# Performance work log

Measured on AMD Instinct MI355X. Metric: run time of the kernel, lower is better.

## Reference

```python
import jax, jax.numpy as jnp
import numpy as np

N_NODES = 100000
N_EDGES = 3200000
FEAT = 16


def gcn_conv(x, src, dst, W, b):
    # PyG GCNConv: add self-loops, symmetric normalization deg^{-1/2}(A+I)deg^{-1/2},
    # then linear transform and scatter-add aggregation.
    n = x.shape[0]
    loop = jnp.arange(n, dtype=src.dtype)
    s = jnp.concatenate([src, loop])
    d = jnp.concatenate([dst, loop])
    deg = jax.ops.segment_sum(jnp.ones_like(d, dtype=x.dtype), d, num_segments=n)
    dinv = jnp.where(deg > 0, jax.lax.rsqrt(deg), 0.0)
    norm = dinv[s] * dinv[d]  # [E+N]
    h = x @ W  # [N, out]
    msg = h[s] * norm[:, None]  # gather + weight
    out = jax.ops.segment_sum(msg, d, num_segments=n)  # scatter-add
    return out + b


def setup_inputs() -> dict:
    key = jax.random.key(0)
    k1, k2, k3, k4 = jax.random.split(key, 4)
    scale = 1.0 / np.sqrt(FEAT)
    return {
        "x": jax.random.normal(k1, (N_NODES, FEAT), dtype=jnp.float32),
        "edge_index": jax.random.randint(k2, (2, N_EDGES), 0, N_NODES, dtype=jnp.int64) if jax.config.jax_enable_x64 else jax.random.randint(k2, (2, N_EDGES), 0, N_NODES, dtype=jnp.int32),
        "W1": jax.random.normal(k3, (FEAT, 16), dtype=jnp.float32) * scale,
        "b1": jnp.zeros((16,), dtype=jnp.float32),
        "W2": jax.random.normal(k4, (16, FEAT), dtype=jnp.float32) * scale,
        "b2": jnp.zeros((FEAT,), dtype=jnp.float32),
    }


def reference(x, edge_index, W1, b1, W2, b2):
    src, dst = edge_index[0], edge_index[1]
    h = gcn_conv(x, src, dst, W1, b1)
    h = jax.nn.relu(h)
    out = gcn_conv(h, src, dst, W2, b2)
    return out
```

## Files before the change

### kernel.cpp

```cpp
#include <hip/hip_runtime.h>

#define F 16
#define BSHIFT 8
#define NPB 256
#define NB 391
#define CH 4096
#define BCAP 9216


__global__ void init_cursor_kernel(unsigned* __restrict__ cursor) {
    int i = threadIdx.x;
    if (i < NB) cursor[i * 16] = (unsigned)(i * BCAP);
}

__global__ __launch_bounds__(512) void
reorder_kernel(const int* __restrict__ src, const int* __restrict__ dst,
               unsigned* __restrict__ cursor, unsigned* __restrict__ recs, int E) {
    __shared__ unsigned lsorted[CH];
    __shared__ unsigned short lbkt[CH];
    __shared__ unsigned cnt[NB];
    __shared__ unsigned lstart[NB + 1];
    int t = threadIdx.x, b = blockIdx.x;
    int e0 = b * CH;
    int cnt_e = E - e0; if (cnt_e > CH) cnt_e = CH;

    for (int i = t; i < NB; i += 512) cnt[i] = 0;
    __syncthreads();
    unsigned pk[8], rs[8];
#pragma unroll
    for (int j = 0; j < 8; ++j) {
        int i = t + j * 512;
        pk[j] = 0xFFFFFFFFu;
        if (i < cnt_e) {
            unsigned d = (unsigned)dst[e0 + i];
            rs[j] = (unsigned)src[e0 + i];
            unsigned bk = d >> BSHIFT;
            unsigned r = atomicAdd(&cnt[bk], 1u);
            pk[j] = bk | ((d & 255u) << 9) | (r << 17);
        }
    }
    __syncthreads();
    if (t < 64) {
        unsigned run = 0;
        for (int c = 0; c < NB; c += 64) {
            int idx = c + t;
            unsigned v = (idx < NB) ? cnt[idx] : 0u;
            unsigned inc = v;
#pragma unroll
            for (int d = 1; d < 64; d <<= 1) {
                unsigned o = __shfl_up(inc, d, 64);
                if (t >= d) inc += o;
            }
            if (idx < NB) lstart[idx] = run + inc - v;
            run += __shfl(inc, 63, 64);
        }
        if (t == 0) lstart[NB] = (unsigned)cnt_e;
    }
    __syncthreads();
    {
        int s0 = (int)(((unsigned)b * 101u) % (unsigned)NB);
        for (int q = t; q < NB; q += 512) {
            int i = s0 + q; if (i >= NB) i -= NB;
            unsigned c = cnt[i];
            if (c) cnt[i] = atomicAdd(&cursor[i * 16], c);
        }
    }
    __syncthreads();
#pragma unroll
    for (int j = 0; j < 8; ++j) {
        int i = t + j * 512;
        if (i < cnt_e) {
            unsigned p = pk[j];
            unsigned bk = p & 0x1FFu;
            unsigned pos = lstart[bk] + (p >> 17);
            lsorted[pos] = rs[j] | (((p >> 9) & 255u) << 17);
            lbkt[pos] = (unsigned short)bk;
        }
    }
    __syncthreads();
    for (int i = t; i < cnt_e; i += 512) {
        unsigned bk = lbkt[i];
        recs[cnt[bk] + ((unsigned)i - lstart[bk])] = lsorted[i];
    }
}

__global__ __launch_bounds__(1024) void
sort2_kernel(const unsigned* __restrict__ recs, const unsigned* __restrict__ cursor,
             unsigned* __restrict__ srcs,
             int* __restrict__ noffA, int* __restrict__ nendA,
             int* __restrict__ noffB, int* __restrict__ nendB,
             float* __restrict__ dinv, const float* __restrict__ x,
             float* __restrict__ z, int n) {
    __shared__ unsigned lsort[BCAP];
    __shared__ unsigned cnt[2 * NPB];
    __shared__ unsigned ex[2 * NPB];
    __shared__ float ldv[NPB];
    __shared__ unsigned wtot[8];
    int t = threadIdx.x, b = blockIdx.x;
    int e0 = b * BCAP;
    int used = (int)(cursor[b * 16] - (unsigned)e0);
    unsigned NH = ((unsigned)n + 1u) >> 1;
    if (t < 2 * NPB) cnt[t] = 0;
    __syncthreads();
    unsigned pk[9], rsr[9];
#pragma unroll
    for (int j = 0; j < 9; ++j) {
        int i = t + j * 1024;
        pk[j] = 0xFFFFFFFFu;
        if (i < used) {
            unsigned rec = recs[e0 + i];
            unsigned node = rec >> 17;
            unsigned half = ((rec & 0x1FFFFu) >= NH) ? 1u : 0u;
            unsigned bin = (half << 8) | node;
            rsr[j] = rec;
            unsigned r = atomicAdd(&cnt[bin], 1u);
            pk[j] = bin | (r << 9);
        }
    }
    __syncthreads();
    {
        unsigned c = 0, inc = 0;
        int lane = t & 63, w = t >> 6;
        if (t < 2 * NPB) {
            c = cnt[t];
            inc = c;
#pragma unroll
            for (int d = 1; d < 64; d <<= 1) {
                unsigned o = __shfl_up(inc, d, 64);
                if (lane >= d) inc += o;
            }
            if (lane == 63) wtot[w] = inc;
        }
        __syncthreads();
        if (t < 2 * NPB) {
            unsigned wbase = 0;
            for (int i = 0; i < w; ++i) wbase += wtot[i];
            unsigned e = wbase + inc - c;
            ex[t] = e;
            int node = t & 255, half = t >> 8;
            int gnode = b * NPB + node;
            if (gnode < n) {
                if (half == 0) { noffA[gnode] = e0 + (int)e; nendA[gnode] = e0 + (int)(e + c); }
                else           { noffB[gnode] = e0 + (int)e; nendB[gnode] = e0 + (int)(e + c); }
            }
        }
        __syncthreads();
    }
    if (t < NPB) {
        unsigned ctot = cnt[t] + cnt[NPB + t];
        float dv = rsqrtf((float)ctot + 1.0f);
        ldv[t] = dv;
        int gnode = b * NPB + t;
        if (gnode < n) dinv[gnode] = dv;
    }
    __syncthreads();
#pragma unroll
    for (int j = 0; j < 9; ++j) {
        int i = t + j * 1024;
        if (i < used) {
            unsigned p = pk[j];
            lsort[ex[p & 511u] + (p >> 9)] = rsr[j];
        }
    }
    __syncthreads();
    for (int i = t; i < used; i += 1024) srcs[e0 + i] = lsort[i];
    {
        int node = b * NPB + (t >> 2);
        if (node < n) {
            float4 v = ((const float4*)x)[(size_t)b * 1024 + t];
            float dv = ldv[t >> 2];
            v.x *= dv; v.y *= dv; v.z *= dv; v.w *= dv;
            ((float4*)z)[(size_t)b * 1024 + t] = v;
        }
    }
}

__global__ __launch_bounds__(256) void
agg_bal_kernel(const float* __restrict__ hin, const unsigned* __restrict__ srcs,
               const int* __restrict__ noffA, const int* __restrict__ nendA,
               const int* __restrict__ noffB, const int* __restrict__ nendB,
               const float* __restrict__ dinv,
               const float* __restrict__ W, const float* __restrict__ bias,
               float* __restrict__ outp, int n, int mode) {
    __shared__ float acc[64][F + 1];
    __shared__ float Ws[F * F];
    int t = threadIdx.x, b = blockIdx.x;
    int g = t >> 2, c = t & 3;
    Ws[t] = W[t];
    for (int i = t; i < 64 * (F + 1); i += 256) ((float*)acc)[i] = 0.f;
    __syncthreads();
    int nfirst = b * 64;
    int nlast = nfirst + 63; if (nlast > n - 1) nlast = n - 1;
    int rs0 = noffA[nfirst], re0 = nendA[nlast];
    int rs1 = noffB[nfirst], re1 = nendB[nlast];
    const float4* h4 = (const float4*)hin;

#define PROC(r, v)                                                        \
    {                                                                     \
        int nd = (int)((r >> 17) & 63u);                                  \
        if (nd != cur) {                                                  \
            float* a = &acc[cur][c * 4];                                  \
            atomicAdd(a + 0, s.x); atomicAdd(a + 1, s.y);                 \
            atomicAdd(a + 2, s.z); atomicAdd(a + 3, s.w);                 \
            s.x = 0.f; s.y = 0.f; s.z = 0.f; s.w = 0.f;                   \
            cur = nd;                                                     \
        }                                                                 \
        s.x += v.x; s.y += v.y; s.z += v.z; s.w += v.w;                   \
    }

#pragma unroll 1
    for (int p = 0; p < 2; ++p) {
        int S = p ? rs1 : rs0;
        int Eend = p ? re1 : re0;
        int T = Eend - S;
        int chunk = (T + 63) >> 6;
        int gs = S + g * chunk;
        int ge = gs + chunk; if (ge > Eend) ge = Eend;
        if (gs < ge) {
            int cur = (int)((srcs[gs] >> 17) & 63u);
            float4 s = {0.f, 0.f, 0.f, 0.f};
            int e = gs;
            for (; e + 4 <= ge; e += 4) {
                unsigned r0 = srcs[e], r1 = srcs[e + 1], r2 = srcs[e + 2], r3 = srcs[e + 3];
                float4 v0 = h4[(size_t)(r0 & 0x1FFFFu) * 4 + c];
                float4 v1 = h4[(size_t)(r1 & 0x1FFFFu) * 4 + c];
                float4 v2 = h4[(size_t)(r2 & 0x1FFFFu) * 4 + c];
                float4 v3 = h4[(size_t)(r3 & 0x1FFFFu) * 4 + c];
                PROC(r0, v0); PROC(r1, v1); PROC(r2, v2); PROC(r3, v3);
            }
            for (; e < ge; ++e) {
                unsigned r0 = srcs[e];
                float4 v0 = h4[(size_t)(r0 & 0x1FFFFu) * 4 + c];
                PROC(r0, v0);
            }
            float* a = &acc[cur][c * 4];
            atomicAdd(a + 0, s.x); atomicAdd(a + 1, s.y);
            atomicAdd(a + 2, s.z); atomicAdd(a + 3, s.w);
        }
        __syncthreads();
    }
#undef PROC
    int node = nfirst + g;
    if (node < n) {
        float4 self = h4[(size_t)node * 4 + c];
        float* ar = &acc[g][c * 4];
        ar[0] += self.x; ar[1] += self.y; ar[2] += self.z; ar[3] += self.w;
    }
    __syncthreads();
    if (node < n) {
        float di = dinv[node];
        float4 o = {0.f, 0.f, 0.f, 0.f};
        int j = c * 4;
#pragma unroll
        for (int k = 0; k < F; ++k) {
            float ak = acc[g][k];
            o.x += ak * Ws[k * F + j + 0];
            o.y += ak * Ws[k * F + j + 1];
            o.z += ak * Ws[k * F + j + 2];
            o.w += ak * Ws[k * F + j + 3];
        }
        float4 bi = ((const float4*)bias)[c];
        o.x = di * o.x + bi.x; o.y = di * o.y + bi.y;
        o.z = di * o.z + bi.z; o.w = di * o.w + bi.w;
        if (mode == 1) {
            o.x = fmaxf(o.x, 0.f) * di; o.y = fmaxf(o.y, 0.f) * di;
            o.z = fmaxf(o.z, 0.f) * di; o.w = fmaxf(o.w, 0.f) * di;
        }
        ((float4*)outp)[(size_t)node * 4 + c] = o;
    }
}


__global__ void deg_kernel(const int* __restrict__ dst, float* __restrict__ deg, int E) {
    int e = blockIdx.x * blockDim.x + threadIdx.x;
    if (e < E) atomicAdd(&deg[dst[e]], 1.0f);
}
__global__ void dinv_kernel(float* __restrict__ deg, int n) {
    int i = blockIdx.x * blockDim.x + threadIdx.x;
    if (i < n) deg[i] = rsqrtf(deg[i] + 1.0f);
}
__global__ void linear2_kernel(const float* __restrict__ in, const float* __restrict__ acc,
                               const float* __restrict__ dinv, const float* __restrict__ W,
                               const float* __restrict__ bias, float* __restrict__ out,
                               int n, int mode) {
    __shared__ float Ws[F * F];
    __shared__ float As[16][F + 1];
    int t = threadIdx.x;
    Ws[t] = W[t];
    int nb = t >> 4, j = t & 15;
    int i = blockIdx.x * 16 + nb;
    float di = 0.f, v = 0.f;
    if (i < n) {
        di = dinv[i]; v = in[i * F + j];
        if (mode) { v = di * (acc[i * F + j] + v) + bias[j]; v = fmaxf(v, 0.f); }
    }
    As[nb][j] = v;
    __syncthreads();
    if (i < n) {
        float s = 0.f;
#pragma unroll
        for (int k = 0; k < F; ++k) s += As[nb][k] * Ws[k * F + j];
        out[i * F + j] = s * di;
    }
}
__global__ void scatter_kernel(const int* __restrict__ src, const int* __restrict__ dst,
                               const float* __restrict__ h, float* __restrict__ acc, int E) {
    int t = blockIdx.x * blockDim.x + threadIdx.x;
    int e = t >> 4, j = t & 15;
    if (e < E) atomicAdd(&acc[dst[e] * F + j], h[src[e] * F + j]);
}
__global__ void out_kernel(const float* __restrict__ acc, const float* __restrict__ h,
                           const float* __restrict__ dinv, const float* __restrict__ bias,
                           float* __restrict__ out, int n) {
    int t = blockIdx.x * blockDim.x + threadIdx.x;
    if (t < n * F) {
        int i = t >> 4, j = t & 15;
        out[t] = dinv[i] * (acc[t] + h[t]) + bias[j];
    }
}


extern "C" void kernel_launch(void* const* d_in, const int* in_sizes, int n_in,
                              void* d_out, int out_size, void* d_ws, size_t ws_size,
                              hipStream_t stream) {
    const float* x  = (const float*)d_in[0];
    const int*   ei = (const int*)d_in[1];
    const float* W1 = (const float*)d_in[2];
    const float* b1 = (const float*)d_in[3];
    const float* W2 = (const float*)d_in[4];
    const float* b2 = (const float*)d_in[5];
    float* outp = (float*)d_out;

    const int N = in_sizes[0] / F;
    const int E = in_sizes[1] / 2;
    const int* src = ei;
    const int* dst = ei + E;

    const int nb_rt = (N + NPB - 1) >> BSHIFT;
    const size_t RC = (size_t)NB * BCAP;
    size_t need = sizeof(unsigned) * ((size_t)N * 21 + 2 * RC + 16 * NB);

    if (nb_rt == NB && E <= CH * 65535 && ws_size >= need) {
        float* dinv = (float*)d_ws;
        float* z = dinv + N;
        unsigned* recs = (unsigned*)(z + (size_t)F * N);
        float* y = (float*)recs;
        unsigned* srcs = recs + RC;
        int* noffA = (int*)(srcs + RC);
        int* nendA = noffA + N;
        int* noffB = nendA + N;
        int* nendB = noffB + N;
        unsigned* cursor = (unsigned*)(nendB + N);

        init_cursor_kernel<<<1, 512, 0, stream>>>(cursor);
        reorder_kernel<<<(E + CH - 1) / CH, 512, 0, stream>>>(src, dst, cursor, recs, E);
        sort2_kernel<<<NB, 1024, 0, stream>>>(recs, cursor, srcs, noffA, nendA, noffB, nendB, dinv, x, z, N);
        agg_bal_kernel<<<(N + 63) / 64, 256, 0, stream>>>(z, srcs, noffA, nendA, noffB, nendB, dinv, W1, b1, y, N, 1);
        agg_bal_kernel<<<(N + 63) / 64, 256, 0, stream>>>(y, srcs, noffA, nendA, noffB, nendB, dinv, W2, b2, outp, N, 2);
    } else {
        float* dinv = (float*)d_ws;
        float* h = dinv + N;
        float* acc = h + (size_t)F * N;
        hipMemsetAsync(dinv, 0, (size_t)N * sizeof(float), stream);
        hipMemsetAsync(acc, 0, (size_t)F * N * sizeof(float), stream);
        deg_kernel<<<(E + 255) / 256, 256, 0, stream>>>(dst, dinv, E);
        dinv_kernel<<<(N + 255) / 256, 256, 0, stream>>>(dinv, N);
        linear2_kernel<<<(N + 15) / 16, 256, 0, stream>>>(x, nullptr, dinv, W1, nullptr, h, N, 0);
        scatter_kernel<<<((size_t)E * F + 255) / 256, 256, 0, stream>>>(src, dst, h, acc, E);
        linear2_kernel<<<(N + 15) / 16, 256, 0, stream>>>(h, acc, dinv, W2, b1, h, N, 1);
        hipMemsetAsync(acc, 0, (size_t)F * N * sizeof(float), stream);
        scatter_kernel<<<((size_t)E * F + 255) / 256, 256, 0, stream>>>(src, dst, h, acc, E);
        out_kernel<<<((size_t)N * F + 255) / 256, 256, 0, stream>>>(acc, h, dinv, b2, outp, N);
    }
}
```

Baseline: 205.1 us.

## Shrink destination buckets to 64 nodes and unroll gather loop by eight

Destination buckets shrink from 256 to 64 nodes (1563 buckets with 2304-slot capacity). The record packing and the sort2 kernel change to match, so each sort2 block uses 512 threads with smaller shared-memory histograms, which should raise occupancy and parallelism in the sort phase. The aggregation kernel gains an 8-way unrolled gather loop to keep more loads in flight. The cost is more buckets, and so more global cursor atomics and more scattered writes in the reorder pass. The smaller per-bucket capacity also leaves less headroom for skewed degree distributions.

```diff
diff --git a/kernel.cpp b/kernel.cpp
--- a/kernel.cpp
+++ b/kernel.cpp
@@ -1,15 +1,15 @@
 #include <hip/hip_runtime.h>
 
 #define F 16
-#define BSHIFT 8
-#define NPB 256
-#define NB 391
+#define BSHIFT 6
+#define NPB 64
+#define NB 1563
 #define CH 4096
-#define BCAP 9216
+#define BCAP 2304
 
 
 __global__ void init_cursor_kernel(unsigned* __restrict__ cursor) {
-    int i = threadIdx.x;
+    int i = blockIdx.x * 512 + threadIdx.x;
     if (i < NB) cursor[i * 16] = (unsigned)(i * BCAP);
 }
 
@@ -36,7 +36,7 @@
             rs[j] = (unsigned)src[e0 + i];
             unsigned bk = d >> BSHIFT;
             unsigned r = atomicAdd(&cnt[bk], 1u);
-            pk[j] = bk | ((d & 255u) << 9) | (r << 17);
+            pk[j] = bk | ((d & 63u) << 11) | (r << 17);
         }
     }
     __syncthreads();
@@ -71,9 +71,9 @@
         int i = t + j * 512;
         if (i < cnt_e) {
             unsigned p = pk[j];
-            unsigned bk = p & 0x1FFu;
+            unsigned bk = p & 0x7FFu;
             unsigned pos = lstart[bk] + (p >> 17);
-            lsorted[pos] = rs[j] | (((p >> 9) & 255u) << 17);
+            lsorted[pos] = rs[j] | (((p >> 11) & 63u) << 17);
             lbkt[pos] = (unsigned short)bk;
         }
     }
@@ -84,7 +84,7 @@
     }
 }
 
-__global__ __launch_bounds__(1024) void
+__global__ __launch_bounds__(512) void
 sort2_kernel(const unsigned* __restrict__ recs, const unsigned* __restrict__ cursor,
              unsigned* __restrict__ srcs,
              int* __restrict__ noffA, int* __restrict__ nendA,
@@ -92,36 +92,36 @@
              float* __restrict__ dinv, const float* __restrict__ x,
              float* __restrict__ z, int n) {
     __shared__ unsigned lsort[BCAP];
-    __shared__ unsigned cnt[2 * NPB];
-    __shared__ unsigned ex[2 * NPB];
+    __shared__ unsigned cnt[128];
+    __shared__ unsigned ex[128];
     __shared__ float ldv[NPB];
-    __shared__ unsigned wtot[8];
+    __shared__ unsigned wtot[2];
     int t = threadIdx.x, b = blockIdx.x;
     int e0 = b * BCAP;
     int used = (int)(cursor[b * 16] - (unsigned)e0);
     unsigned NH = ((unsigned)n + 1u) >> 1;
-    if (t < 2 * NPB) cnt[t] = 0;
-    __syncthreads();
-    unsigned pk[9], rsr[9];
-#pragma unroll
-    for (int j = 0; j < 9; ++j) {
-        int i = t + j * 1024;
+    if (t < 128) cnt[t] = 0;
+    __syncthreads();
+    unsigned pk[5], rsr[5];
+#pragma unroll
+    for (int j = 0; j < 5; ++j) {
+        int i = t + j * 512;
         pk[j] = 0xFFFFFFFFu;
         if (i < used) {
             unsigned rec = recs[e0 + i];
             unsigned node = rec >> 17;
             unsigned half = ((rec & 0x1FFFFu) >= NH) ? 1u : 0u;
-            unsigned bin = (half << 8) | node;
+            unsigned bin = (half << 6) | node;
             rsr[j] = rec;
             unsigned r = atomicAdd(&cnt[bin], 1u);
-            pk[j] = bin | (r << 9);
+            pk[j] = bin | (r << 7);
         }
     }
     __syncthreads();
     {
         unsigned c = 0, inc = 0;
         int lane = t & 63, w = t >> 6;
-        if (t < 2 * NPB) {
+        if (t < 128) {
             c = cnt[t];
             inc = c;
 #pragma unroll
@@ -132,22 +132,21 @@
             if (lane == 63) wtot[w] = inc;
         }
         __syncthreads();
-        if (t < 2 * NPB) {
-            unsigned wbase = 0;
-            for (int i = 0; i < w; ++i) wbase += wtot[i];
-            unsigned e = wbase + inc - c;
+        if (t < 128) {
+            unsigned base = (w == 1) ? wtot[0] : 0u;
+            unsigned e = base + inc - c;
             ex[t] = e;
-            int node = t & 255, half = t >> 8;
+            int node = t & 63, half = t >> 6;
             int gnode = b * NPB + node;
             if (gnode < n) {
                 if (half == 0) { noffA[gnode] = e0 + (int)e; nendA[gnode] = e0 + (int)(e + c); }
                 else           { noffB[gnode] = e0 + (int)e; nendB[gnode] = e0 + (int)(e + c); }
             }
         }
-        __syncthreads();
-    }
+    }
+    __syncthreads();
     if (t < NPB) {
-        unsigned ctot = cnt[t] + cnt[NPB + t];
+        unsigned ctot = cnt[t] + cnt[64 + t];
         float dv = rsqrtf((float)ctot + 1.0f);
         ldv[t] = dv;
         int gnode = b * NPB + t;
@@ -155,22 +154,22 @@
     }
     __syncthreads();
 #pragma unroll
-    for (int j = 0; j < 9; ++j) {
-        int i = t + j * 1024;
+    for (int j = 0; j < 5; ++j) {
+        int i = t + j * 512;
         if (i < used) {
             unsigned p = pk[j];
-            lsort[ex[p & 511u] + (p >> 9)] = rsr[j];
-        }
-    }
-    __syncthreads();
-    for (int i = t; i < used; i += 1024) srcs[e0 + i] = lsort[i];
-    {
+            lsort[ex[p & 127u] + (p >> 7)] = rsr[j];
+        }
+    }
+    __syncthreads();
+    for (int i = t; i < used; i += 512) srcs[e0 + i] = lsort[i];
+    if (t < NPB * 4) {
         int node = b * NPB + (t >> 2);
         if (node < n) {
-            float4 v = ((const float4*)x)[(size_t)b * 1024 + t];
+            float4 v = ((const float4*)x)[(size_t)b * (NPB * 4) + t];
             float dv = ldv[t >> 2];
             v.x *= dv; v.y *= dv; v.z *= dv; v.w *= dv;
-            ((float4*)z)[(size_t)b * 1024 + t] = v;
+            ((float4*)z)[(size_t)b * (NPB * 4) + t] = v;
         }
     }
 }
@@ -220,6 +219,22 @@
             int cur = (int)((srcs[gs] >> 17) & 63u);
             float4 s = {0.f, 0.f, 0.f, 0.f};
             int e = gs;
+            for (; e + 8 <= ge; e += 8) {
+                unsigned r0 = srcs[e + 0], r1 = srcs[e + 1];
+                unsigned r2 = srcs[e + 2], r3 = srcs[e + 3];
+                unsigned r4 = srcs[e + 4], r5 = srcs[e + 5];
+                unsigned r6 = srcs[e + 6], r7 = srcs[e + 7];
+                float4 v0 = h4[(size_t)(r0 & 0x1FFFFu) * 4 + c];
+                float4 v1 = h4[(size_t)(r1 & 0x1FFFFu) * 4 + c];
+                float4 v2 = h4[(size_t)(r2 & 0x1FFFFu) * 4 + c];
+                float4 v3 = h4[(size_t)(r3 & 0x1FFFFu) * 4 + c];
+                float4 v4 = h4[(size_t)(r4 & 0x1FFFFu) * 4 + c];
+                float4 v5 = h4[(size_t)(r5 & 0x1FFFFu) * 4 + c];
+                float4 v6 = h4[(size_t)(r6 & 0x1FFFFu) * 4 + c];
+                float4 v7 = h4[(size_t)(r7 & 0x1FFFFu) * 4 + c];
+                PROC(r0, v0); PROC(r1, v1); PROC(r2, v2); PROC(r3, v3);
+                PROC(r4, v4); PROC(r5, v5); PROC(r6, v6); PROC(r7, v7);
+            }
             for (; e + 4 <= ge; e += 4) {
                 unsigned r0 = srcs[e], r1 = srcs[e + 1], r2 = srcs[e + 2], r3 = srcs[e + 3];
                 float4 v0 = h4[(size_t)(r0 & 0x1FFFFu) * 4 + c];
@@ -352,11 +367,11 @@
         int* nendB = noffB + N;
         unsigned* cursor = (unsigned*)(nendB + N);
 
-        init_cursor_kernel<<<1, 512, 0, stream>>>(cursor);
+        init_cursor_kernel<<<(NB + 511) / 512, 512, 0, stream>>>(cursor);
         reorder_kernel<<<(E + CH - 1) / CH, 512, 0, stream>>>(src, dst, cursor, recs, E);
-        sort2_kernel<<<NB, 1024, 0, stream>>>(recs, cursor, srcs, noffA, nendA, noffB, nendB, dinv, x, z, N);
-        agg_bal_kernel<<<(N + 63) / 64, 256, 0, stream>>>(z, srcs, noffA, nendA, noffB, nendB, dinv, W1, b1, y, N, 1);
-        agg_bal_kernel<<<(N + 63) / 64, 256, 0, stream>>>(y, srcs, noffA, nendA, noffB, nendB, dinv, W2, b2, outp, N, 2);
+        sort2_kernel<<<NB, 512, 0, stream>>>(recs, cursor, srcs, noffA, nendA, noffB, nendB, dinv, x, z, N);
+        agg_bal_kernel<<<NB, 256, 0, stream>>>(z, srcs, noffA, nendA, noffB, nendB, dinv, W1, b1, y, N, 1);
+        agg_bal_kernel<<<NB, 256, 0, stream>>>(y, srcs, noffA, nendA, noffB, nendB, dinv, W2, b2, outp, N, 2);
     } else {
         float* dinv = (float*)d_ws;
         float* h = dinv + N;
```

New measurement: 254.8 us. +24.3%, slower.

## Split sort2 buckets across two blocks and deepen gather unroll

Applied to the files above, without the earlier changes.

The second-level sort kernel now launches two 512-thread blocks per bucket, each handling half of the bucket's 256 nodes. Each block re-scans the bucket's records twice and places them with atomic cursor increments instead of register-held ranks, using half-sized shared memory. The intent is more blocks and better occupancy for this phase, at the cost of reading every record twice per half. The order of edges within a node becomes nondeterministic, and a fixed HCAP of 4608 per half could overflow on a skewed split. Separately, the aggregation gather loop gets an 8-wide unrolled stage to keep more loads in flight.

```diff
diff --git a/kernel.cpp b/kernel.cpp
--- a/kernel.cpp
+++ b/kernel.cpp
@@ -6,6 +6,7 @@
 #define NB 391
 #define CH 4096
 #define BCAP 9216
+#define HCAP 4608
 
 
 __global__ void init_cursor_kernel(unsigned* __restrict__ cursor) {
@@ -84,44 +85,40 @@
     }
 }
 
-__global__ __launch_bounds__(1024) void
+__global__ __launch_bounds__(512) void
 sort2_kernel(const unsigned* __restrict__ recs, const unsigned* __restrict__ cursor,
              unsigned* __restrict__ srcs,
              int* __restrict__ noffA, int* __restrict__ nendA,
              int* __restrict__ noffB, int* __restrict__ nendB,
              float* __restrict__ dinv, const float* __restrict__ x,
              float* __restrict__ z, int n) {
-    __shared__ unsigned lsort[BCAP];
-    __shared__ unsigned cnt[2 * NPB];
-    __shared__ unsigned ex[2 * NPB];
-    __shared__ float ldv[NPB];
-    __shared__ unsigned wtot[8];
+    __shared__ unsigned lsort[HCAP];
+    __shared__ unsigned cnt[256];
+    __shared__ unsigned ex[256];
+    __shared__ float ldv[128];
+    __shared__ unsigned wtot[4];
+    __shared__ unsigned tot_s;
     int t = threadIdx.x, b = blockIdx.x;
-    int e0 = b * BCAP;
-    int used = (int)(cursor[b * 16] - (unsigned)e0);
+    int bucket = b >> 1, h = b & 1;
+    int e0 = bucket * BCAP;
+    int o0 = b * HCAP;
+    int used = (int)(cursor[bucket * 16] - (unsigned)e0);
     unsigned NH = ((unsigned)n + 1u) >> 1;
-    if (t < 2 * NPB) cnt[t] = 0;
-    __syncthreads();
-    unsigned pk[9], rsr[9];
-#pragma unroll
-    for (int j = 0; j < 9; ++j) {
-        int i = t + j * 1024;
-        pk[j] = 0xFFFFFFFFu;
-        if (i < used) {
-            unsigned rec = recs[e0 + i];
-            unsigned node = rec >> 17;
-            unsigned half = ((rec & 0x1FFFFu) >= NH) ? 1u : 0u;
-            unsigned bin = (half << 8) | node;
-            rsr[j] = rec;
-            unsigned r = atomicAdd(&cnt[bin], 1u);
-            pk[j] = bin | (r << 9);
+    if (t < 256) cnt[t] = 0;
+    __syncthreads();
+    for (int i = t; i < used; i += 512) {
+        unsigned rec = recs[e0 + i];
+        unsigned node = rec >> 17;
+        if ((int)(node >> 7) == h) {
+            unsigned bin = (((rec & 0x1FFFFu) >= NH) ? 128u : 0u) | (node & 127u);
+            atomicAdd(&cnt[bin], 1u);
         }
     }
     __syncthreads();
     {
         unsigned c = 0, inc = 0;
         int lane = t & 63, w = t >> 6;
-        if (t < 2 * NPB) {
+        if (t < 256) {
             c = cnt[t];
             inc = c;
 #pragma unroll
@@ -132,45 +129,49 @@
             if (lane == 63) wtot[w] = inc;
         }
         __syncthreads();
-        if (t < 2 * NPB) {
+        if (t < 256) {
             unsigned wbase = 0;
             for (int i = 0; i < w; ++i) wbase += wtot[i];
             unsigned e = wbase + inc - c;
             ex[t] = e;
-            int node = t & 255, half = t >> 8;
-            int gnode = b * NPB + node;
+            if (t == 255) tot_s = e + c;
+            int half = t >> 7, nl = t & 127;
+            int gnode = bucket * NPB + h * 128 + nl;
             if (gnode < n) {
-                if (half == 0) { noffA[gnode] = e0 + (int)e; nendA[gnode] = e0 + (int)(e + c); }
-                else           { noffB[gnode] = e0 + (int)e; nendB[gnode] = e0 + (int)(e + c); }
-            }
-        }
-        __syncthreads();
-    }
-    if (t < NPB) {
-        unsigned ctot = cnt[t] + cnt[NPB + t];
+                if (half == 0) { noffA[gnode] = o0 + (int)e; nendA[gnode] = o0 + (int)(e + c); }
+                else           { noffB[gnode] = o0 + (int)e; nendB[gnode] = o0 + (int)(e + c); }
+            }
+        }
+    }
+    __syncthreads();
+    if (t < 128) {
+        unsigned ctot = cnt[t] + cnt[128 + t];
         float dv = rsqrtf((float)ctot + 1.0f);
         ldv[t] = dv;
-        int gnode = b * NPB + t;
+        int gnode = bucket * NPB + h * 128 + t;
         if (gnode < n) dinv[gnode] = dv;
     }
     __syncthreads();
-#pragma unroll
-    for (int j = 0; j < 9; ++j) {
-        int i = t + j * 1024;
-        if (i < used) {
-            unsigned p = pk[j];
-            lsort[ex[p & 511u] + (p >> 9)] = rsr[j];
-        }
-    }
-    __syncthreads();
-    for (int i = t; i < used; i += 1024) srcs[e0 + i] = lsort[i];
+    for (int i = t; i < used; i += 512) {
+        unsigned rec = recs[e0 + i];
+        unsigned node = rec >> 17;
+        if ((int)(node >> 7) == h) {
+            unsigned bin = (((rec & 0x1FFFFu) >= NH) ? 128u : 0u) | (node & 127u);
+            unsigned pos = atomicAdd(&ex[bin], 1u);
+            lsort[pos] = rec;
+        }
+    }
+    __syncthreads();
+    int tot = (int)tot_s;
+    for (int i = t; i < tot; i += 512) srcs[o0 + i] = lsort[i];
     {
-        int node = b * NPB + (t >> 2);
-        if (node < n) {
-            float4 v = ((const float4*)x)[(size_t)b * 1024 + t];
-            float dv = ldv[t >> 2];
+        int nl = t >> 2;
+        int gnode = bucket * NPB + h * 128 + nl;
+        if (gnode < n) {
+            float4 v = ((const float4*)x)[(size_t)gnode * 4 + (t & 3)];
+            float dv = ldv[nl];
             v.x *= dv; v.y *= dv; v.z *= dv; v.w *= dv;
-            ((float4*)z)[(size_t)b * 1024 + t] = v;
+            ((float4*)z)[(size_t)gnode * 4 + (t & 3)] = v;
         }
     }
 }
@@ -220,6 +221,22 @@
             int cur = (int)((srcs[gs] >> 17) & 63u);
             float4 s = {0.f, 0.f, 0.f, 0.f};
             int e = gs;
+            for (; e + 8 <= ge; e += 8) {
+                unsigned r0 = srcs[e + 0], r1 = srcs[e + 1];
+                unsigned r2 = srcs[e + 2], r3 = srcs[e + 3];
+                unsigned r4 = srcs[e + 4], r5 = srcs[e + 5];
+                unsigned r6 = srcs[e + 6], r7 = srcs[e + 7];
+                float4 v0 = h4[(size_t)(r0 & 0x1FFFFu) * 4 + c];
+                float4 v1 = h4[(size_t)(r1 & 0x1FFFFu) * 4 + c];
+                float4 v2 = h4[(size_t)(r2 & 0x1FFFFu) * 4 + c];
+                float4 v3 = h4[(size_t)(r3 & 0x1FFFFu) * 4 + c];
+                float4 v4 = h4[(size_t)(r4 & 0x1FFFFu) * 4 + c];
+                float4 v5 = h4[(size_t)(r5 & 0x1FFFFu) * 4 + c];
+                float4 v6 = h4[(size_t)(r6 & 0x1FFFFu) * 4 + c];
+                float4 v7 = h4[(size_t)(r7 & 0x1FFFFu) * 4 + c];
+                PROC(r0, v0); PROC(r1, v1); PROC(r2, v2); PROC(r3, v3);
+                PROC(r4, v4); PROC(r5, v5); PROC(r6, v6); PROC(r7, v7);
+            }
             for (; e + 4 <= ge; e += 4) {
                 unsigned r0 = srcs[e], r1 = srcs[e + 1], r2 = srcs[e + 2], r3 = srcs[e + 3];
                 float4 v0 = h4[(size_t)(r0 & 0x1FFFFu) * 4 + c];
@@ -354,7 +371,7 @@
 
         init_cursor_kernel<<<1, 512, 0, stream>>>(cursor);
         reorder_kernel<<<(E + CH - 1) / CH, 512, 0, stream>>>(src, dst, cursor, recs, E);
-        sort2_kernel<<<NB, 1024, 0, stream>>>(recs, cursor, srcs, noffA, nendA, noffB, nendB, dinv, x, z, N);
+        sort2_kernel<<<NB * 2, 512, 0, stream>>>(recs, cursor, srcs, noffA, nendA, noffB, nendB, dinv, x, z, N);
         agg_bal_kernel<<<(N + 63) / 64, 256, 0, stream>>>(z, srcs, noffA, nendA, noffB, nendB, dinv, W1, b1, y, N, 1);
         agg_bal_kernel<<<(N + 63) / 64, 256, 0, stream>>>(y, srcs, noffA, nendA, noffB, nendB, dinv, W2, b2, outp, N, 2);
     } else {
```

Measured after the change: 209.9 us. 1.02x slower.
